# Performance work log

Measured on AMD Instinct MI355X. Metric: run time of the kernel, lower is better.

Reference implementation:

```python
import jax, jax.numpy as jnp
import numpy as np

H = 64   # hid_dim (hard-coded in Attn_LSTM)
C = 8    # enc_in / out_dim
L = 96   # enc_seq_len = interval*lag = max_length
T = 24   # pre_len = window*horizon
B = 4096


def _p(key, shape, scale=0.1):
    return (jax.random.normal(key, shape, dtype=jnp.float32) * scale)


def setup_inputs() -> dict:
    key = jax.random.key(0)
    ks = jax.random.split(key, 20)
    inp = {
        'x_enc': jax.random.normal(ks[0], (B, L, C), dtype=jnp.float32),
        'x_mark_enc': jax.random.normal(ks[1], (B, L, 4), dtype=jnp.float32),
        'x_dec': jax.random.normal(ks[2], (B, T, C), dtype=jnp.float32),
        'x_mark_dec': jax.random.normal(ks[3], (B, T, 4), dtype=jnp.float32),
        # encoder LSTM (1 layer, input C -> hid H), pytorch gate order i,f,g,o
        'enc_Wih': _p(ks[4], (4 * H, C)), 'enc_Whh': _p(ks[5], (4 * H, H)),
        'enc_bih': _p(ks[6], (4 * H,)), 'enc_bhh': _p(ks[7], (4 * H,)),
        # decoder
        'emb_W': _p(ks[8], (H, C)), 'emb_b': _p(ks[9], (H,)),
        'attn_W': _p(ks[10], (L, 2 * H)), 'attn_b': _p(ks[11], (L,)),
        'comb_W': _p(ks[12], (H, 2 * H)), 'comb_b': _p(ks[13], (H,)),
        'dec_Wih': _p(ks[14], (4 * H, H)), 'dec_Whh': _p(ks[15], (4 * H, H)),
        'dec_bih': _p(ks[16], (4 * H,)), 'dec_bhh': _p(ks[17], (4 * H,)),
        'out_W': _p(ks[18], (C, H)), 'out_b': _p(ks[19], (C,)),
    }
    return inp


def _lstm_cell(x, h, c, Wih, Whh, bih, bhh):
    g = x @ Wih.T + h @ Whh.T + (bih + bhh)
    i, f, gg, o = jnp.split(g, 4, axis=-1)
    i, f, o = jax.nn.sigmoid(i), jax.nn.sigmoid(f), jax.nn.sigmoid(o)
    c_new = f * c + i * jnp.tanh(gg)
    h_new = o * jnp.tanh(c_new)
    return h_new, c_new


def _forward(x_enc, enc_Wih, enc_Whh, enc_bih, enc_bhh,
             emb_W, emb_b, attn_W, attn_b, comb_W, comb_b,
             dec_Wih, dec_Whh, dec_bih, dec_bhh, out_W, out_b):
    seq_last = x_enc[:, -1:, :]               # [B,1,C]
    x = x_enc - seq_last                      # normalized

    # ---- encoder: 1-layer LSTM over L steps ----
    h0 = jnp.zeros((x.shape[0], H), dtype=x.dtype)
    c0 = jnp.zeros_like(h0)

    def enc_step(carry, xt):
        h, c = carry
        h, c = _lstm_cell(xt, h, c, enc_Wih, enc_Whh, enc_bih, enc_bhh)
        return (h, c), h

    (h_enc, c_enc), enc_out = jax.lax.scan(enc_step, (h0, c0),
                                           jnp.swapaxes(x, 0, 1))
    enc_out = jnp.swapaxes(enc_out, 0, 1)     # [B,L,H]

    # ---- attention decoder: T sequential steps ----
    dec_in0 = x[:, -1, :]                     # last (normalized) input, [B,C]

    def dec_step(carry, _):
        inp, h, c = carry
        emb = jax.nn.relu(inp @ emb_W.T + emb_b)                       # [B,H]
        aw = jax.nn.softmax(jnp.concatenate([emb, h], -1) @ attn_W.T + attn_b)  # [B,L]
        ctx = jnp.einsum('bl,blh->bh', aw, enc_out)                    # [B,H]
        comb = jnp.concatenate([emb, ctx], -1) @ comb_W.T + comb_b     # [B,H]
        h, c = _lstm_cell(comb, h, c, dec_Wih, dec_Whh, dec_bih, dec_bhh)
        pred = h @ out_W.T + out_b                                     # [B,C]
        # original code feeds prediction.detach() back in
        return (jax.lax.stop_gradient(pred), h, c), (pred, aw)

    _, (preds, aws) = jax.lax.scan(dec_step, (dec_in0, h_enc, c_enc),
                                   None, length=T)
    pre_y = jnp.swapaxes(preds, 0, 1) + seq_last   # [B,T,C]
    return pre_y


def reference(x_enc, x_mark_enc, x_dec, x_mark_dec,
              enc_Wih, enc_Whh, enc_bih, enc_bhh,
              emb_W, emb_b, attn_W, attn_b, comb_W, comb_b,
              dec_Wih, dec_Whh, dec_bih, dec_bhh, out_W, out_b):
    # x_mark_enc, x_dec, x_mark_dec are accepted but unused (as in original)
    return _forward(x_enc, enc_Wih, enc_Whh, enc_bih, enc_bhh,
                    emb_W, emb_b, attn_W, attn_b, comb_W, comb_b,
                    dec_Wih, dec_Whh, dec_bih, dec_bhh, out_W, out_b)
```

## Files before the change

kernel.cpp:

```cpp
#include <hip/hip_runtime.h>

#define LL 96
#define TT 24
#define HH 64
#define CC 8
#define GG 256
#define BT 8
#define NB 512

typedef unsigned short u16t;
typedef unsigned int   u32t;
typedef __attribute__((ext_vector_type(8))) short bf16x8;
typedef __attribute__((ext_vector_type(4))) float f32x4;

__device__ __forceinline__ float b2f(u16t u){ union{u32t i; float f;} v; v.i=((u32t)u)<<16; return v.f; }
__device__ __forceinline__ u16t f2b(float f){ union{float f; u32t i;} v; v.f=f; u32t l=(v.i>>16)&1u; v.i+=0x7fffu+l; return (u16t)(v.i>>16); }
__device__ __forceinline__ float rcpf(float x){ return __builtin_amdgcn_rcpf(x); }
__device__ __forceinline__ float sigm(float x){ return rcpf(1.f + __expf(-x)); }
__device__ __forceinline__ float tanh2(float x){ return 1.f - 2.f*rcpf(__expf(2.f*x) + 1.f); }
__device__ __forceinline__ u32t pk2(float a, float b){ return (u32t)f2b(a) | ((u32t)f2b(b)<<16); }
__device__ __forceinline__ bf16x8 u2b8(uint4 u){ union{uint4 a; bf16x8 b;} v; v.a=u; return v.b; }
__device__ __forceinline__ int aaddr(int k, int m){ return (((k>>5)*4 + ((k>>3)&3))*16 + m)*8 + (k&7); }

__device__ __forceinline__ void bar_lds(){
    asm volatile("s_waitcnt lgkmcnt(0)" ::: "memory");
    __builtin_amdgcn_s_barrier();
    asm volatile("" ::: "memory");
    __builtin_amdgcn_sched_barrier(0);
}

template<bool F32> __device__ __forceinline__ float ldf(const void* p, size_t i){
    if constexpr (F32) return ((const float*)p)[i];
    else               return b2f(((const u16t*)p)[i]);
}
template<bool F32> __device__ __forceinline__ uint4 ld8p(const void* p, size_t i){
    if constexpr (F32){
        const float* f = (const float*)p + i;
        uint4 r; r.x = pk2(f[0],f[1]); r.y = pk2(f[2],f[3]);
                 r.z = pk2(f[4],f[5]); r.w = pk2(f[6],f[7]);
        return r;
    } else return *(const uint4*)((const u16t*)p + i);
}
template<bool F32> __device__ __forceinline__ void stf(void* p, size_t i, float v){
    if constexpr (F32) ((float*)p)[i] = v;
    else               ((u16t*)p)[i] = f2b(v);
}
template<bool F32> __device__ __forceinline__ float ldW_enc(const void* wih, const void* whh, int r, int k){
    if (k < CC)      return ldf<F32>(wih, (size_t)r*CC + k);
    else if (k < 72) return ldf<F32>(whh, (size_t)r*HH + (k-CC));
    else             return 0.f;
}

__device__ __forceinline__ bool inputs_are_f32(const void* bih){
    const u16t* p = (const u16t*)bih;
    int cnt = 0;
    #pragma unroll
    for (int i = 0; i < 64; ++i){
        u32t e = ((u32t)p[i] >> 7) & 0xFFu;
        cnt += (e >= 128u) ? 1 : 0;
    }
    return cnt > 0;
}

template<bool F32>
__global__ __launch_bounds__(256,4) void enc4_g(
    const void* __restrict__ x_enc,
    const void* __restrict__ eWih, const void* __restrict__ eWhh,
    const void* __restrict__ ebih, const void* __restrict__ ebhh,
    u16t* __restrict__ eoG, float* __restrict__ cG)
{
    if (inputs_are_f32(ebih) != F32) return;

    __shared__ __align__(16) short Abuf2[2][1536];

    const int tid = threadIdx.x;
    const int b0  = blockIdx.x * 4;
    const int col = tid & 15, quad = (tid >> 4) & 3, wv = tid >> 6;

    bf16x8 Bf[4][3];
    float  biasg[4];
    #pragma unroll
    for (int g = 0; g < 4; ++g){
        int r = g*64 + wv*16 + col;
        biasg[g] = ldf<F32>(ebih, r) + ldf<F32>(ebhh, r);
        #pragma unroll
        for (int kb = 0; kb < 3; ++kb){
            bf16x8 v;
            #pragma unroll
            for (int x = 0; x < 8; ++x){
                int k = kb*32 + quad*8 + x;
                v[x] = (short)f2b(ldW_enc<F32>(eWih, eWhh, r, k));
            }
            Bf[g][kb] = v;
        }
    }
    for (int n = tid; n < 2*1536; n += 256) ((short*)Abuf2)[n] = 0;
    float sl = 0.f; size_t xbase = 0;
    if (tid < 32){ int b = tid >> 3, i = tid & 7;
        xbase = (size_t)(b0+b)*(LL*CC) + i;
        sl = ldf<F32>(x_enc, xbase + (size_t)(LL-1)*CC);
    }
    __syncthreads();
    if (tid < 32){ short v = (short)f2b(ldf<F32>(x_enc, xbase) - sl);
        Abuf2[0][tid] = v; Abuf2[0][tid+32] = v; Abuf2[0][tid+64] = v; Abuf2[0][tid+96] = v; }
    float xr = (tid < 32) ? ldf<F32>(x_enc, xbase + CC) : 0.f;

    const int jmy = wv*16 + col;
    const int hwbase = aaddr(8 + jmy, 0);
    const u32t ebase = ((u32t)(b0 + quad)*4u + (u32t)(jmy>>4))*1536u + (u32t)((jmy&15)*8);

    float creg = 0.f;
    u32t  pkv  = 0;

    #pragma unroll 2
    for (int t = 0; t < LL; ++t){
        bar_lds();
        const bf16x8* AbR = (const bf16x8*)Abuf2[t & 1];
        short*        AbW = Abuf2[(t + 1) & 1];
        bf16x8 a0 = AbR[(0*4 + quad)*16 + col];
        bf16x8 a1 = AbR[(1*4 + quad)*16 + col];
        bf16x8 a2 = AbR[(2*4 + quad)*16 + col];
        f32x4 acc[4];
        #pragma unroll
        for (int g = 0; g < 4; ++g){
            f32x4 a; a[0]=biasg[g]; a[1]=biasg[g]; a[2]=biasg[g]; a[3]=biasg[g];
            a = __builtin_amdgcn_mfma_f32_16x16x32_bf16(a0, Bf[g][0], a, 0,0,0);
            a = __builtin_amdgcn_mfma_f32_16x16x32_bf16(a1, Bf[g][1], a, 0,0,0);
            a = __builtin_amdgcn_mfma_f32_16x16x32_bf16(a2, Bf[g][2], a, 0,0,0);
            acc[g] = a;
        }
        float c = sigm(acc[1][quad])*creg + sigm(acc[0][quad])*tanh2(acc[2][quad]);
        float h = sigm(acc[3][quad])*tanh2(c);
        creg = c;
        u16t hb = f2b(h);
        if ((t & 1) == 0) pkv = hb;
        else {
            pkv |= ((u32t)hb) << 16;
            *(u32t*)&eoG[ebase + (u32t)((t>>5)*512 + ((t>>3)&3)*128 + (t&7) - 1)] = pkv;
        }
        AbW[hwbase + quad*8]      = (short)hb;
        AbW[hwbase + quad*8+32]   = (short)hb;
        AbW[hwbase + quad*8+64]   = (short)hb;
        AbW[hwbase + quad*8+96]   = (short)hb;
        if (tid < 32 && t < LL-1){
            short v = (short)f2b(xr - sl);
            AbW[tid] = v; AbW[tid+32] = v; AbW[tid+64] = v; AbW[tid+96] = v;
            int tn = (t+2 < LL) ? t+2 : LL-1;
            xr = ldf<F32>(x_enc, xbase + (size_t)tn*CC);
        }
    }
    cG[(size_t)(b0 + quad)*HH + jmy] = creg;
}

template<bool F32>
__global__ __launch_bounds__(256,2) void dec8_g(
    const void* __restrict__ x_enc,
    const void* __restrict__ embW, const void* __restrict__ embb,
    const void* __restrict__ attnW, const void* __restrict__ attnb,
    const void* __restrict__ combW, const void* __restrict__ combb,
    const void* __restrict__ dWih, const void* __restrict__ dWhh,
    const void* __restrict__ dbih, const void* __restrict__ dbhh,
    const void* __restrict__ outW, const void* __restrict__ outb,
    void* __restrict__ outp, const u16t* __restrict__ eoG,
    const float* __restrict__ cG)
{
    if (inputs_are_f32(dbih) != F32) return;

    __shared__ __align__(16) float slp[CC*10];
    __shared__ __align__(16) char  uni[17184];
    __shared__ __align__(16) u16t BaL[6*4*4*16*8];
    __shared__ __align__(16) u16t M1L[64*64];
    __shared__ __align__(16) u16t oWL[8*64];

    const int tid = threadIdx.x;
    const int b0  = blockIdx.x * BT;
    const int col = tid & 15, quad = (tid >> 4) & 3, wv = tid >> 6;
    const int r0  = (quad >> 1) * 2;
    const int jmy = wv*16 + col;

    if (tid < BT*CC){ int b = tid >> 3, i = tid & 7;
        slp[i*10 + b] = ldf<F32>(x_enc, (size_t)(b0+b)*(LL*CC) + (size_t)(LL-1)*CC + i); }

    bf16x8 Bd[4][4];
    #pragma unroll
    for (int g = 0; g < 4; ++g){
        int r = g*64 + wv*16 + col;
        Bd[g][0] = u2b8(ld8p<F32>(dWih, (size_t)r*HH + quad*8));
        Bd[g][1] = u2b8(ld8p<F32>(dWih, (size_t)r*HH + 32 + quad*8));
        Bd[g][2] = u2b8(ld8p<F32>(dWhh, (size_t)r*HH + quad*8));
        Bd[g][3] = u2b8(ld8p<F32>(dWhh, (size_t)r*HH + 32 + quad*8));
    }
    bf16x8 Bc[4];
    #pragma unroll
    for (int kb = 0; kb < 4; ++kb)
        Bc[kb] = u2b8(ld8p<F32>(combW, (size_t)(wv*16+col)*128 + kb*32 + quad*8));
    bf16x8 zz = {0,0,0,0,0,0,0,0};

    for (int idx = tid; idx < 1536; idx += 256){
        int lt_ = idx >> 8, kb_ = (idx >> 6) & 3, q_ = (idx >> 4) & 3, c_ = idx & 15;
        int row = lt_*16 + c_;
        u16t tmp[8];
        #pragma unroll
        for (int x = 0; x < 8; ++x)
            tmp[x] = f2b(ldf<F32>(attnW, (size_t)row*128 + kb_*32 + q_*8 + x));
        *(uint4*)&BaL[(size_t)idx*8] = *(uint4*)tmp;
    }
    for (int idx = tid; idx < 1024; idx += 256){
        int j = idx >> 4, k0 = (idx & 15) * 4;
        float acc4[4] = {0.f,0.f,0.f,0.f};
        #pragma unroll
        for (int c = 0; c < 8; ++c){
            float e = ldf<F32>(embW, (size_t)j*CC + c);
            #pragma unroll
            for (int kk = 0; kk < 4; ++kk)
                acc4[kk] += e * ldf<F32>(outW, (size_t)c*HH + k0 + kk);
        }
        u16t tmp[4];
        #pragma unroll
        for (int kk = 0; kk < 4; ++kk) tmp[kk] = f2b(acc4[kk]);
        int sw = (((k0 >> 3) ^ (j & 7)) << 3) | (k0 & 7);
        *(uint2*)&M1L[j*64 + sw] = *(uint2*)tmp;
    }
    for (int n = tid; n < 512; n += 256){
        int c = n >> 6, k = n & 63;
        int sw = (((k >> 3) ^ (c & 7)) << 3) | (k & 7);
        oWL[c*64 + sw] = f2b(ldf<F32>(outW, n));
    }

    float* decB  = (float*)(uni + 0);
    float* attnB = (float*)(uni + 1024);
    float* b1B   = (float*)(uni + 1408);
    float* combB = (float*)(uni + 1664);
    float* outB  = (float*)(uni + 1920);
    float* Lg    = (float*)(uni + 1952);
    u16t*  awB   = (u16t*)(uni + 5408);
    u16t*  Ae    = (u16t*)(uni + 6944);
    u16t*  Ah0   = (u16t*)(uni + 8992);
    u16t*  Ah1   = (u16t*)(uni + 11040);
    u16t*  Actx  = (u16t*)(uni + 13088);
    u16t*  Acmb  = (u16t*)(uni + 15136);

    float creg[2];
    #pragma unroll
    for (int rr = 0; rr < 2; ++rr){
        int b = (quad*4 + r0 + rr) & 7;
        u16t hv = eoG[(((size_t)(b0+b)*4 + (size_t)(jmy>>4))*3 + 2)*512 + 3*128 + (jmy&15)*8 + 7];
        Ah0[aaddr(jmy, b)]   = hv;
        Ah0[aaddr(jmy, b+8)] = hv;
        creg[rr] = cG[(size_t)(b0+b)*HH + jmy];
    }
    decB[tid] = ldf<F32>(dbih, tid) + ldf<F32>(dbhh, tid);
    if (tid < LL) attnB[tid] = ldf<F32>(attnb, tid);
    if (tid < HH){
        float s = ldf<F32>(embb, tid);
        #pragma unroll
        for (int c = 0; c < 8; ++c)
            s += ldf<F32>(embW, (size_t)tid*CC + c) * ldf<F32>(outb, c);
        b1B[tid] = s;
    }
    if (tid < HH) combB[tid] = ldf<F32>(combb, tid);
    if (tid < CC) outB[tid]  = ldf<F32>(outb, tid);
    {
        float e0v = fmaxf(ldf<F32>(embb, jmy), 0.f);
        u16t ev = f2b(e0v);
        #pragma unroll
        for (int r = 0; r < 4; ++r)
            Ae[aaddr(jmy, quad*4 + r)] = ev;
    }
    __syncthreads();

    const u16t* ebp = eoG + (size_t)(b0 + wv*2) * 6144;
    uint4 eF0[12], eF1[12];
    #pragma unroll
    for (int f = 0; f < 12; ++f) eF0[f] = *(const uint4*)(ebp + f*512 + quad*128 + col*8);
    #pragma unroll
    for (int f = 0; f < 12; ++f) eF1[f] = *(const uint4*)(ebp + 6144 + f*512 + quad*128 + col*8);

    const int lgS = tid & 31, bS = tid >> 5;
    const bf16x8* AeV   = (const bf16x8*)Ae;
    const bf16x8* ActxV = (const bf16x8*)Actx;
    const bf16x8* AcmbV = (const bf16x8*)Acmb;

    for (int t = 0; t < TT; ++t){
        u16t* AhR = (t & 1) ? Ah1 : Ah0;
        u16t* AhW = (t & 1) ? Ah0 : Ah1;
        const bf16x8* AhV = (const bf16x8*)AhR;

        {
            bf16x8 ae0 = AeV[(0*4+quad)*16 + col], ae1 = AeV[(1*4+quad)*16 + col];
            bf16x8 ah0 = AhV[(0*4+quad)*16 + col], ah1 = AhV[(1*4+quad)*16 + col];
            const int ns = (wv < 2) ? 2 : 1;
            for (int s = 0; s < ns; ++s){
                int lt = (s == 0) ? wv : 4+wv;
                const u16t* bp = &BaL[lt*2048 + quad*128 + col*8];
                float bz = attnB[lt*16 + col];
                f32x4 a; a[0]=bz; a[1]=bz; a[2]=bz; a[3]=bz;
                a = __builtin_amdgcn_mfma_f32_16x16x32_bf16(ae0, *(const bf16x8*)&bp[0],    a, 0,0,0);
                a = __builtin_amdgcn_mfma_f32_16x16x32_bf16(ae1, *(const bf16x8*)&bp[512],  a, 0,0,0);
                a = __builtin_amdgcn_mfma_f32_16x16x32_bf16(ah0, *(const bf16x8*)&bp[1024], a, 0,0,0);
                a = __builtin_amdgcn_mfma_f32_16x16x32_bf16(ah1, *(const bf16x8*)&bp[1536], a, 0,0,0);
                if (quad < 2){
                    int rb = (lt*16+col)*9 + quad*4;
                    Lg[rb+0] = a[0]; Lg[rb+1] = a[1]; Lg[rb+2] = a[2]; Lg[rb+3] = a[3];
                }
            }
        }
        bar_lds();

        {
            int l = lgS*3;
            float e0 = __expf(Lg[l*9 + bS]), e1 = __expf(Lg[(l+1)*9 + bS]), e2 = __expf(Lg[(l+2)*9 + bS]);
            float sm = e0 + e1 + e2;
            #pragma unroll
            for (int m = 16; m >= 1; m >>= 1) sm += __shfl_xor(sm, m, 32);
            float inv = rcpf(sm);
            awB[bS*96 + l]     = f2b(e0*inv);
            awB[bS*96 + l + 1] = f2b(e1*inv);
            awB[bS*96 + l + 2] = f2b(e2*inv);
        }
        {
            const u16t* ap0 = awB + (wv*2)*96;
            bf16x8 f0 = *(const bf16x8*)(ap0 + quad*8);
            bf16x8 f1 = *(const bf16x8*)(ap0 + 32 + quad*8);
            bf16x8 f2 = *(const bf16x8*)(ap0 + 64 + quad*8);
            #pragma unroll
            for (int nt = 0; nt < 4; ++nt){
                f32x4 a; a[0]=0.f; a[1]=0.f; a[2]=0.f; a[3]=0.f;
                a = __builtin_amdgcn_mfma_f32_16x16x32_bf16(f0, u2b8(eF0[nt*3+0]), a, 0,0,0);
                a = __builtin_amdgcn_mfma_f32_16x16x32_bf16(f1, u2b8(eF0[nt*3+1]), a, 0,0,0);
                a = __builtin_amdgcn_mfma_f32_16x16x32_bf16(f2, u2b8(eF0[nt*3+2]), a, 0,0,0);
                if (quad == 0){
                    u16t v = f2b(a[0]);
                    Actx[aaddr(nt*16+col, wv*2)]   = v;
                    Actx[aaddr(nt*16+col, wv*2+8)] = v;
                }
            }
            const u16t* ap1 = awB + (wv*2+1)*96;
            bf16x8 g0 = *(const bf16x8*)(ap1 + quad*8);
            bf16x8 g1 = *(const bf16x8*)(ap1 + 32 + quad*8);
            bf16x8 g2 = *(const bf16x8*)(ap1 + 64 + quad*8);
            #pragma unroll
            for (int nt = 0; nt < 4; ++nt){
                f32x4 a; a[0]=0.f; a[1]=0.f; a[2]=0.f; a[3]=0.f;
                a = __builtin_amdgcn_mfma_f32_16x16x32_bf16(g0, u2b8(eF1[nt*3+0]), a, 0,0,0);
                a = __builtin_amdgcn_mfma_f32_16x16x32_bf16(g1, u2b8(eF1[nt*3+1]), a, 0,0,0);
                a = __builtin_amdgcn_mfma_f32_16x16x32_bf16(g2, u2b8(eF1[nt*3+2]), a, 0,0,0);
                if (quad == 0){
                    u16t v = f2b(a[0]);
                    Actx[aaddr(nt*16+col, wv*2+1)] = v;
                    Actx[aaddr(nt*16+col, wv*2+9)] = v;
                }
            }
        }
        bar_lds();

        {
            bf16x8 ae0 = AeV[(0*4+quad)*16 + col],   ae1 = AeV[(1*4+quad)*16 + col];
            bf16x8 ax0 = ActxV[(0*4+quad)*16 + col], ax1 = ActxV[(1*4+quad)*16 + col];
            float bz = combB[wv*16 + col];
            f32x4 a; a[0]=bz; a[1]=bz; a[2]=bz; a[3]=bz;
            a = __builtin_amdgcn_mfma_f32_16x16x32_bf16(ae0, Bc[0], a, 0,0,0);
            a = __builtin_amdgcn_mfma_f32_16x16x32_bf16(ae1, Bc[1], a, 0,0,0);
            a = __builtin_amdgcn_mfma_f32_16x16x32_bf16(ax0, Bc[2], a, 0,0,0);
            a = __builtin_amdgcn_mfma_f32_16x16x32_bf16(ax1, Bc[3], a, 0,0,0);
            #pragma unroll
            for (int r = 0; r < 4; ++r)
                Acmb[aaddr(wv*16+col, quad*4 + r)] = f2b(a[r]);
        }
        bar_lds();

        {
            bf16x8 ac0 = AcmbV[(0*4+quad)*16 + col], ac1 = AcmbV[(1*4+quad)*16 + col];
            bf16x8 ah0 = AhV[(0*4+quad)*16 + col],   ah1 = AhV[(1*4+quad)*16 + col];
            f32x4 g4[4];
            #pragma unroll
            for (int g = 0; g < 4; ++g){
                float bz = decB[g*64 + wv*16 + col];
                f32x4 a; a[0]=bz; a[1]=bz; a[2]=bz; a[3]=bz;
                a = __builtin_amdgcn_mfma_f32_16x16x32_bf16(ac0, Bd[g][0], a, 0,0,0);
                a = __builtin_amdgcn_mfma_f32_16x16x32_bf16(ac1, Bd[g][1], a, 0,0,0);
                a = __builtin_amdgcn_mfma_f32_16x16x32_bf16(ah0, Bd[g][2], a, 0,0,0);
                a = __builtin_amdgcn_mfma_f32_16x16x32_bf16(ah1, Bd[g][3], a, 0,0,0);
                g4[g] = a;
            }
            #pragma unroll
            for (int rr = 0; rr < 2; ++rr){
                int r = r0 + rr;
                int b = (quad*4 + r) & 7;
                float c = sigm(g4[1][r])*creg[rr] + sigm(g4[0][r])*tanh2(g4[2][r]);
                float h = sigm(g4[3][r])*tanh2(c);
                creg[rr] = c;
                u16t hv = f2b(h);
                AhW[aaddr(jmy, b)]   = hv;
                AhW[aaddr(jmy, b+8)] = hv;
            }
        }
        bar_lds();

        {
            const bf16x8* AhWV = (const bf16x8*)AhW;
            bf16x8 xh0 = AhWV[(0*4+quad)*16 + col];
            bf16x8 xh1 = AhWV[(1*4+quad)*16 + col];
            bf16x8 m10 = *(const bf16x8*)&M1L[jmy*64 + ((quad ^ (jmy&7))<<3)];
            bf16x8 m11 = *(const bf16x8*)&M1L[jmy*64 + (((4+quad) ^ (jmy&7))<<3)];
            float eb = b1B[wv*16 + col];
            f32x4 a; a[0]=eb; a[1]=eb; a[2]=eb; a[3]=eb;
            a = __builtin_amdgcn_mfma_f32_16x16x32_bf16(xh0, m10, a, 0,0,0);
            a = __builtin_amdgcn_mfma_f32_16x16x32_bf16(xh1, m11, a, 0,0,0);
            #pragma unroll
            for (int r = 0; r < 4; ++r)
                Ae[aaddr(wv*16+col, quad*4 + r)] = f2b(fmaxf(a[r], 0.f));
            if (wv == 3){
                bf16x8 oBf0 = zz, oBf1 = zz;
                if (col < CC){
                    oBf0 = *(const bf16x8*)&oWL[col*64 + ((quad ^ col)<<3)];
                    oBf1 = *(const bf16x8*)&oWL[col*64 + (((4+quad) ^ col)<<3)];
                }
                float ob = outB[col & 7];
                f32x4 p4; p4[0]=ob; p4[1]=ob; p4[2]=ob; p4[3]=ob;
                p4 = __builtin_amdgcn_mfma_f32_16x16x32_bf16(xh0, oBf0, p4, 0,0,0);
                p4 = __builtin_amdgcn_mfma_f32_16x16x32_bf16(xh1, oBf1, p4, 0,0,0);
                if (col < CC){
                    #pragma unroll
                    for (int r = 0; r < 4; ++r){
                        int m = quad*4 + r;
                        if (m < 8)
                            stf<F32>(outp, ((size_t)(b0+m)*TT + t)*CC + col, p4[r] + slp[col*10 + m]);
                    }
                }
            }
        }
        bar_lds();
    }
}

template<bool F32>
__global__ __launch_bounds__(256,2) void fused_g(
    const void* __restrict__ x_enc,
    const void* __restrict__ eWih, const void* __restrict__ eWhh,
    const void* __restrict__ ebih, const void* __restrict__ ebhh,
    const void* __restrict__ embW, const void* __restrict__ embb,
    const void* __restrict__ attnW, const void* __restrict__ attnb,
    const void* __restrict__ combW, const void* __restrict__ combb,
    const void* __restrict__ dWih, const void* __restrict__ dWhh,
    const void* __restrict__ dbih, const void* __restrict__ dbhh,
    const void* __restrict__ outW, const void* __restrict__ outb,
    void* __restrict__ outp, u16t* __restrict__ eoG)
{
    if (inputs_are_f32(ebih) != F32) return;

    __shared__ __align__(16) float slp[CC*10];
    __shared__ __align__(16) short Abuf2[2][1536];
    __shared__ __align__(16) char  uni[18880];

    const int tid = threadIdx.x;
    const int b0  = blockIdx.x * BT;
    const int col = tid & 15, quad = (tid >> 4) & 3, wv = tid >> 6;
    const int r0  = (quad >> 1) * 2;

    bf16x8 Bf[4][3];
    float  biasg[4];
    #pragma unroll
    for (int g = 0; g < 4; ++g){
        int r = g*64 + wv*16 + col;
        biasg[g] = ldf<F32>(ebih, r) + ldf<F32>(ebhh, r);
        #pragma unroll
        for (int kb = 0; kb < 3; ++kb){
            bf16x8 v;
            #pragma unroll
            for (int x = 0; x < 8; ++x){
                int k = kb*32 + quad*8 + x;
                v[x] = (short)f2b(ldW_enc<F32>(eWih, eWhh, r, k));
            }
            Bf[g][kb] = v;
        }
    }
    for (int n = tid; n < 2*1536; n += 256) ((short*)Abuf2)[n] = 0;
    float sl = 0.f; size_t xbase = 0;
    if (tid < BT*CC){ int b = tid >> 3, i = tid & 7;
        xbase = (size_t)(b0+b)*(LL*CC) + i;
        sl = ldf<F32>(x_enc, xbase + (size_t)(LL-1)*CC);
        slp[i*10 + b] = sl; }
    __syncthreads();
    if (tid < BT*CC){ short v = (short)f2b(ldf<F32>(x_enc, xbase) - sl);
        Abuf2[0][tid] = v; Abuf2[0][tid + 64] = v; }
    float xr = (tid < BT*CC) ? ldf<F32>(x_enc, xbase + CC) : 0.f;

    const int jmy = wv*16 + col;
    const int kh  = 8 + jmy;
    const int hwbase = aaddr(kh, 0);

    u32t ebase[2];
    #pragma unroll
    for (int rr = 0; rr < 2; ++rr){
        u32t bg = (u32t)(b0 + ((quad*4 + r0 + rr) & 7));
        ebase[rr] = (bg*4u + (u32t)(jmy>>4))*1536u + (u32t)((jmy&15)*8);
    }

    float creg[2] = {0.f,0.f};
    u16t  hb16[2] = {0,0};

    for (int t = 0; t < LL; ++t){
        __syncthreads();
        const bf16x8* AbR = (const bf16x8*)Abuf2[t & 1];
        short*        AbW = Abuf2[(t + 1) & 1];
        bf16x8 a0 = AbR[(0*4 + quad)*16 + col];
        bf16x8 a1 = AbR[(1*4 + quad)*16 + col];
        bf16x8 a2 = AbR[(2*4 + quad)*16 + col];
        f32x4 acc[4];
        #pragma unroll
        for (int g = 0; g < 4; ++g){
            f32x4 a; a[0]=biasg[g]; a[1]=biasg[g]; a[2]=biasg[g]; a[3]=biasg[g];
            a = __builtin_amdgcn_mfma_f32_16x16x32_bf16(a0, Bf[g][0], a, 0,0,0);
            a = __builtin_amdgcn_mfma_f32_16x16x32_bf16(a1, Bf[g][1], a, 0,0,0);
            a = __builtin_amdgcn_mfma_f32_16x16x32_bf16(a2, Bf[g][2], a, 0,0,0);
            acc[g] = a;
        }
        int off = (t>>5)*512 + ((t>>3)&3)*128 + (t&7);
        #pragma unroll
        for (int rr = 0; rr < 2; ++rr){
            int r = r0 + rr;
            int b = (quad*4 + r) & 7;
            float c = sigm(acc[1][r])*creg[rr] + sigm(acc[0][r])*tanh2(acc[2][r]);
            float h = sigm(acc[3][r])*tanh2(c);
            creg[rr] = c; hb16[rr] = f2b(h);
            eoG[ebase[rr] + off] = hb16[rr];
            AbW[hwbase + b*8]     = (short)hb16[rr];
            AbW[hwbase + (b+8)*8] = (short)hb16[rr];
        }
        if (tid < BT*CC && t < LL-1){
            short v = (short)f2b(xr - sl);
            AbW[tid] = v; AbW[tid + 64] = v;
            int tn = (t+2 < LL) ? t+2 : LL-1;
            xr = ldf<F32>(x_enc, xbase + (size_t)tn*CC);
        }
    }

    bf16x8 Bd[4][4];
    #pragma unroll
    for (int g = 0; g < 4; ++g){
        int r = g*64 + wv*16 + col;
        Bd[g][0] = u2b8(ld8p<F32>(dWih, (size_t)r*HH + quad*8));
        Bd[g][1] = u2b8(ld8p<F32>(dWih, (size_t)r*HH + 32 + quad*8));
        Bd[g][2] = u2b8(ld8p<F32>(dWhh, (size_t)r*HH + quad*8));
        Bd[g][3] = u2b8(ld8p<F32>(dWhh, (size_t)r*HH + 32 + quad*8));
    }
    bf16x8 Ba[2][4];
    #pragma unroll
    for (int kb = 0; kb < 4; ++kb)
        Ba[0][kb] = u2b8(ld8p<F32>(attnW, (size_t)(wv*16+col)*128 + kb*32 + quad*8));
    if (wv < 2){
        #pragma unroll
        for (int kb = 0; kb < 4; ++kb)
            Ba[1][kb] = u2b8(ld8p<F32>(attnW, (size_t)((4+wv)*16+col)*128 + kb*32 + quad*8));
    } else {
        #pragma unroll
        for (int kb = 0; kb < 4; ++kb) Ba[1][kb] = Ba[0][kb];
    }
    bf16x8 Bc[4];
    #pragma unroll
    for (int kb = 0; kb < 4; ++kb)
        Bc[kb] = u2b8(ld8p<F32>(combW, (size_t)(wv*16+col)*128 + kb*32 + quad*8));
    bf16x8 zz = {0,0,0,0,0,0,0,0};
    bf16x8 eBf = zz;
    if (quad == 0) eBf = u2b8(ld8p<F32>(embW, (size_t)(wv*16+col)*CC));
    bf16x8 oBf0 = zz, oBf1 = zz;
    if (col < CC){
        oBf0 = u2b8(ld8p<F32>(outW, (size_t)col*HH + quad*8));
        oBf1 = u2b8(ld8p<F32>(outW, (size_t)col*HH + 32 + quad*8));
    }

    float* decB  = (float*)(uni + 0);
    float* attnB = (float*)(uni + 1024);
    float* embB  = (float*)(uni + 1408);
    float* combB = (float*)(uni + 1664);
    float* outB  = (float*)(uni + 1920);
    float* Lg    = (float*)(uni + 1952);
    u16t*  awB   = (u16t*)(uni + 5024);
    u16t*  Ae    = (u16t*)(uni + 6560);
    u16t*  Ah0   = (u16t*)(uni + 8608);
    u16t*  Ah1   = (u16t*)(uni + 10656);
    u16t*  Actx  = (u16t*)(uni + 12704);
    u16t*  Acmb  = (u16t*)(uni + 14752);
    u16t*  Apred = (u16t*)(uni + 16800);

    #pragma unroll
    for (int rr = 0; rr < 2; ++rr){
        int b = (quad*4 + r0 + rr) & 7;
        Ah0[aaddr(jmy, b)]     = hb16[rr];
        Ah0[aaddr(jmy, b+8)]   = hb16[rr];
    }
    decB[tid] = ldf<F32>(dbih, tid) + ldf<F32>(dbhh, tid);
    if (tid < LL) attnB[tid] = ldf<F32>(attnb, tid);
    if (tid < HH) embB[tid]  = ldf<F32>(embb, tid);
    if (tid < HH) combB[tid] = ldf<F32>(combb, tid);
    if (tid < CC) outB[tid]  = ldf<F32>(outb, tid);
    for (int n = tid; n < 1024; n += 256) Apred[n] = 0;
    __syncthreads();

    const u16t* ebp = eoG + (size_t)(b0 + wv*2) * 6144;
    uint4 eF0[12], eF1[12];
    #pragma unroll
    for (int f = 0; f < 12; ++f) eF0[f] = *(const uint4*)(ebp + f*512 + quad*128 + col*8);
    #pragma unroll
    for (int f = 0; f < 12; ++f) eF1[f] = *(const uint4*)(ebp + 6144 + f*512 + quad*128 + col*8);

    const int lgS = tid & 31, bS = tid >> 5;
    const bf16x8* AeV   = (const bf16x8*)Ae;
    const bf16x8* ActxV = (const bf16x8*)Actx;
    const bf16x8* AcmbV = (const bf16x8*)Acmb;
    const bf16x8* ApV   = (const bf16x8*)Apred;

    for (int t = 0; t < TT; ++t){
        u16t* AhR = (t & 1) ? Ah1 : Ah0;
        u16t* AhW = (t & 1) ? Ah0 : Ah1;
        const bf16x8* AhV = (const bf16x8*)AhR;

        {
            bf16x8 ap = ApV[quad*16 + col];
            float eb = embB[wv*16 + col];
            f32x4 a; a[0]=eb; a[1]=eb; a[2]=eb; a[3]=eb;
            a = __builtin_amdgcn_mfma_f32_16x16x32_bf16(ap, eBf, a, 0,0,0);
            #pragma unroll
            for (int r = 0; r < 4; ++r)
                Ae[aaddr(wv*16+col, quad*4 + r)] = f2b(fmaxf(a[r], 0.f));
        }
        __syncthreads();

        {
            bf16x8 ae0 = AeV[(0*4+quad)*16 + col], ae1 = AeV[(1*4+quad)*16 + col];
            bf16x8 ah0 = AhV[(0*4+quad)*16 + col], ah1 = AhV[(1*4+quad)*16 + col];
            const int ns = (wv < 2) ? 2 : 1;
            for (int s = 0; s < ns; ++s){
                int lt = (s == 0) ? wv : 4+wv;
                float bz = attnB[lt*16 + col];
                f32x4 a; a[0]=bz; a[1]=bz; a[2]=bz; a[3]=bz;
                a = __builtin_amdgcn_mfma_f32_16x16x32_bf16(ae0, Ba[s][0], a, 0,0,0);
                a = __builtin_amdgcn_mfma_f32_16x16x32_bf16(ae1, Ba[s][1], a, 0,0,0);
                a = __builtin_amdgcn_mfma_f32_16x16x32_bf16(ah0, Ba[s][2], a, 0,0,0);
                a = __builtin_amdgcn_mfma_f32_16x16x32_bf16(ah1, Ba[s][3], a, 0,0,0);
                if (quad < 2)
                    *(float4*)&Lg[(lt*16+col)*8 + quad*4] = make_float4(a[0],a[1],a[2],a[3]);
            }
        }
        __syncthreads();

        {
            int l = lgS*3;
            float ev0 = Lg[l*8 + bS], ev1 = Lg[(l+1)*8 + bS], ev2 = Lg[(l+2)*8 + bS];
            float mx = fmaxf(ev0, fmaxf(ev1, ev2));
            #pragma unroll
            for (int m = 16; m >= 1; m >>= 1) mx = fmaxf(mx, __shfl_xor(mx, m, 32));
            float e0 = __expf(ev0 - mx), e1 = __expf(ev1 - mx), e2 = __expf(ev2 - mx);
            float sm = e0 + e1 + e2;
            #pragma unroll
            for (int m = 16; m >= 1; m >>= 1) sm += __shfl_xor(sm, m, 32);
            float inv = rcpf(sm);
            awB[bS*96 + l]     = f2b(e0*inv);
            awB[bS*96 + l + 1] = f2b(e1*inv);
            awB[bS*96 + l + 2] = f2b(e2*inv);
        }
        {
            const u16t* ap0 = awB + (wv*2)*96;
            bf16x8 f0 = *(const bf16x8*)(ap0 + quad*8);
            bf16x8 f1 = *(const bf16x8*)(ap0 + 32 + quad*8);
            bf16x8 f2 = *(const bf16x8*)(ap0 + 64 + quad*8);
            #pragma unroll
            for (int nt = 0; nt < 4; ++nt){
                f32x4 a; a[0]=0.f; a[1]=0.f; a[2]=0.f; a[3]=0.f;
                a = __builtin_amdgcn_mfma_f32_16x16x32_bf16(f0, u2b8(eF0[nt*3+0]), a, 0,0,0);
                a = __builtin_amdgcn_mfma_f32_16x16x32_bf16(f1, u2b8(eF0[nt*3+1]), a, 0,0,0);
                a = __builtin_amdgcn_mfma_f32_16x16x32_bf16(f2, u2b8(eF0[nt*3+2]), a, 0,0,0);
                if (quad == 0){
                    u16t v = f2b(a[0]);
                    Actx[aaddr(nt*16+col, wv*2)]   = v;
                    Actx[aaddr(nt*16+col, wv*2+8)] = v;
                }
            }
            const u16t* ap1 = awB + (wv*2+1)*96;
            bf16x8 g0 = *(const bf16x8*)(ap1 + quad*8);
            bf16x8 g1 = *(const bf16x8*)(ap1 + 32 + quad*8);
            bf16x8 g2 = *(const bf16x8*)(ap1 + 64 + quad*8);
            #pragma unroll
            for (int nt = 0; nt < 4; ++nt){
                f32x4 a; a[0]=0.f; a[1]=0.f; a[2]=0.f; a[3]=0.f;
                a = __builtin_amdgcn_mfma_f32_16x16x32_bf16(g0, u2b8(eF1[nt*3+0]), a, 0,0,0);
                a = __builtin_amdgcn_mfma_f32_16x16x32_bf16(g1, u2b8(eF1[nt*3+1]), a, 0,0,0);
                a = __builtin_amdgcn_mfma_f32_16x16x32_bf16(g2, u2b8(eF1[nt*3+2]), a, 0,0,0);
                if (quad == 0){
                    u16t v = f2b(a[0]);
                    Actx[aaddr(nt*16+col, wv*2+1)] = v;
                    Actx[aaddr(nt*16+col, wv*2+9)] = v;
                }
            }
        }
        __syncthreads();

        {
            bf16x8 ae0 = AeV[(0*4+quad)*16 + col],   ae1 = AeV[(1*4+quad)*16 + col];
            bf16x8 ax0 = ActxV[(0*4+quad)*16 + col], ax1 = ActxV[(1*4+quad)*16 + col];
            float bz = combB[wv*16 + col];
            f32x4 a; a[0]=bz; a[1]=bz; a[2]=bz; a[3]=bz;
            a = __builtin_amdgcn_mfma_f32_16x16x32_bf16(ae0, Bc[0], a, 0,0,0);
            a = __builtin_amdgcn_mfma_f32_16x16x32_bf16(ae1, Bc[1], a, 0,0,0);
            a = __builtin_amdgcn_mfma_f32_16x16x32_bf16(ax0, Bc[2], a, 0,0,0);
            a = __builtin_amdgcn_mfma_f32_16x16x32_bf16(ax1, Bc[3], a, 0,0,0);
            #pragma unroll
            for (int r = 0; r < 4; ++r)
                Acmb[aaddr(wv*16+col, quad*4 + r)] = f2b(a[r]);
        }
        __syncthreads();

        {
            bf16x8 ac0 = AcmbV[(0*4+quad)*16 + col], ac1 = AcmbV[(1*4+quad)*16 + col];
            bf16x8 ah0 = AhV[(0*4+quad)*16 + col],   ah1 = AhV[(1*4+quad)*16 + col];
            f32x4 g4[4];
            #pragma unroll
            for (int g = 0; g < 4; ++g){
                float bz = decB[g*64 + wv*16 + col];
                f32x4 a; a[0]=bz; a[1]=bz; a[2]=bz; a[3]=bz;
                a = __builtin_amdgcn_mfma_f32_16x16x32_bf16(ac0, Bd[g][0], a, 0,0,0);
                a = __builtin_amdgcn_mfma_f32_16x16x32_bf16(ac1, Bd[g][1], a, 0,0,0);
                a = __builtin_amdgcn_mfma_f32_16x16x32_bf16(ah0, Bd[g][2], a, 0,0,0);
                a = __builtin_amdgcn_mfma_f32_16x16x32_bf16(ah1, Bd[g][3], a, 0,0,0);
                g4[g] = a;
            }
            #pragma unroll
            for (int rr = 0; rr < 2; ++rr){
                int r = r0 + rr;
                int b = (quad*4 + r) & 7;
                float c = sigm(g4[1][r])*creg[rr] + sigm(g4[0][r])*tanh2(g4[2][r]);
                float h = sigm(g4[3][r])*tanh2(c);
                creg[rr] = c;
                u16t hv = f2b(h);
                AhW[aaddr(jmy, b)]   = hv;
                AhW[aaddr(jmy, b+8)] = hv;
            }
        }
        __syncthreads();

        if (wv == 0){
            const bf16x8* AhWV = (const bf16x8*)AhW;
            bf16x8 xh0 = AhWV[(0*4+quad)*16 + col];
            bf16x8 xh1 = AhWV[(1*4+quad)*16 + col];
            float ob = outB[col & 7];
            f32x4 a; a[0]=ob; a[1]=ob; a[2]=ob; a[3]=ob;
            a = __builtin_amdgcn_mfma_f32_16x16x32_bf16(xh0, oBf0, a, 0,0,0);
            a = __builtin_amdgcn_mfma_f32_16x16x32_bf16(xh1, oBf1, a, 0,0,0);
            if (col < CC){
                #pragma unroll
                for (int r = 0; r < 4; ++r){
                    int m = quad*4 + r, b = m & 7;
                    float p = a[r];
                    Apred[aaddr(col, m)] = f2b(p);
                    if (m < 8)
                        stf<F32>(outp, ((size_t)(b0+b)*TT + t)*CC + col, p + slp[col*10 + b]);
                }
            }
        }
        __syncthreads();
    }
}

extern "C" void kernel_launch(void* const* d_in, const int* in_sizes, int n_in,
                              void* d_out, int out_size, void* d_ws, size_t ws_size,
                              hipStream_t stream)
{
    (void)out_size;
    bool doBF = true, doF32 = true;
    if (in_sizes && n_in > 6){
        if (in_sizes[6] == 512)  doF32 = false;
        else if (in_sizes[6] == 1024) doBF = false;
    }
    u16t* eoG = (u16t*)d_ws;
    if (ws_size >= 50331648ull + 1048576ull){
        float* cG = (float*)((char*)d_ws + 50331648ull);
        if (doBF){
            enc4_g<false><<<1024, 256, 0, stream>>>(
                d_in[0], d_in[4], d_in[5], d_in[6], d_in[7], eoG, cG);
            dec8_g<false><<<NB, 256, 0, stream>>>(
                d_in[0],
                d_in[8],  d_in[9],  d_in[10], d_in[11],
                d_in[12], d_in[13], d_in[14], d_in[15],
                d_in[16], d_in[17], d_in[18], d_in[19],
                d_out, eoG, cG);
        }
        if (doF32){
            enc4_g<true ><<<1024, 256, 0, stream>>>(
                d_in[0], d_in[4], d_in[5], d_in[6], d_in[7], eoG, cG);
            dec8_g<true ><<<NB, 256, 0, stream>>>(
                d_in[0],
                d_in[8],  d_in[9],  d_in[10], d_in[11],
                d_in[12], d_in[13], d_in[14], d_in[15],
                d_in[16], d_in[17], d_in[18], d_in[19],
                d_out, eoG, cG);
        }
    } else {
        if (doBF)
            fused_g<false><<<NB, 256, 0, stream>>>(
                d_in[0],
                d_in[4],  d_in[5],  d_in[6],  d_in[7],
                d_in[8],  d_in[9],  d_in[10], d_in[11],
                d_in[12], d_in[13], d_in[14], d_in[15],
                d_in[16], d_in[17], d_in[18], d_in[19],
                d_out, eoG);
        if (doF32)
            fused_g<true><<<NB, 256, 0, stream>>>(
                d_in[0],
                d_in[4],  d_in[5],  d_in[6],  d_in[7],
                d_in[8],  d_in[9],  d_in[10], d_in[11],
                d_in[12], d_in[13], d_in[14], d_in[15],
                d_in[16], d_in[17], d_in[18], d_in[19],
                d_out, eoG);
    }
}
```

Measured before the change: 273.8 us.

## Pack 16 batch rows per encoder MFMA tile instead of replicating 4

Result: faster. 252.8 us, median of 2 (-7.7%).

```diff
diff --git a/kernel.cpp b/kernel.cpp
--- a/kernel.cpp
+++ b/kernel.cpp
@@ -63,7 +63,7 @@
 }
 
 template<bool F32>
-__global__ __launch_bounds__(256,4) void enc4_g(
+__global__ __launch_bounds__(256,1) void enc16_g(
     const void* __restrict__ x_enc,
     const void* __restrict__ eWih, const void* __restrict__ eWhh,
     const void* __restrict__ ebih, const void* __restrict__ ebhh,
@@ -74,7 +74,7 @@
     __shared__ __align__(16) short Abuf2[2][1536];
 
     const int tid = threadIdx.x;
-    const int b0  = blockIdx.x * 4;
+    const int b0  = blockIdx.x * 16;
     const int col = tid & 15, quad = (tid >> 4) & 3, wv = tid >> 6;
 
     bf16x8 Bf[4][3];
@@ -96,21 +96,23 @@
     }
     for (int n = tid; n < 2*1536; n += 256) ((short*)Abuf2)[n] = 0;
     float sl = 0.f; size_t xbase = 0;
-    if (tid < 32){ int b = tid >> 3, i = tid & 7;
+    if (tid < 128){ int b = tid >> 3, i = tid & 7;
         xbase = (size_t)(b0+b)*(LL*CC) + i;
         sl = ldf<F32>(x_enc, xbase + (size_t)(LL-1)*CC);
     }
     __syncthreads();
-    if (tid < 32){ short v = (short)f2b(ldf<F32>(x_enc, xbase) - sl);
-        Abuf2[0][tid] = v; Abuf2[0][tid+32] = v; Abuf2[0][tid+64] = v; Abuf2[0][tid+96] = v; }
-    float xr = (tid < 32) ? ldf<F32>(x_enc, xbase + CC) : 0.f;
+    if (tid < 128) Abuf2[0][tid] = (short)f2b(ldf<F32>(x_enc, xbase) - sl);
+    float xr = (tid < 128) ? ldf<F32>(x_enc, xbase + CC) : 0.f;
 
     const int jmy = wv*16 + col;
-    const int hwbase = aaddr(8 + jmy, 0);
-    const u32t ebase = ((u32t)(b0 + quad)*4u + (u32t)(jmy>>4))*1536u + (u32t)((jmy&15)*8);
-
-    float creg = 0.f;
-    u32t  pkv  = 0;
+    const int hwb = aaddr(8 + jmy, 0);
+    u32t ebase[4];
+    #pragma unroll
+    for (int r = 0; r < 4; ++r)
+        ebase[r] = ((u32t)(b0 + quad*4 + r)*4u + (u32t)(jmy>>4))*1536u + (u32t)((jmy&15)*8);
+
+    float creg[4] = {0.f,0.f,0.f,0.f};
+    u32t  pkv[4]  = {0,0,0,0};
 
     #pragma unroll 2
     for (int t = 0; t < LL; ++t){
@@ -129,27 +131,29 @@
             a = __builtin_amdgcn_mfma_f32_16x16x32_bf16(a2, Bf[g][2], a, 0,0,0);
             acc[g] = a;
         }
-        float c = sigm(acc[1][quad])*creg + sigm(acc[0][quad])*tanh2(acc[2][quad]);
-        float h = sigm(acc[3][quad])*tanh2(c);
-        creg = c;
-        u16t hb = f2b(h);
-        if ((t & 1) == 0) pkv = hb;
-        else {
-            pkv |= ((u32t)hb) << 16;
-            *(u32t*)&eoG[ebase + (u32t)((t>>5)*512 + ((t>>3)&3)*128 + (t&7) - 1)] = pkv;
-        }
-        AbW[hwbase + quad*8]      = (short)hb;
-        AbW[hwbase + quad*8+32]   = (short)hb;
-        AbW[hwbase + quad*8+64]   = (short)hb;
-        AbW[hwbase + quad*8+96]   = (short)hb;
-        if (tid < 32 && t < LL-1){
-            short v = (short)f2b(xr - sl);
-            AbW[tid] = v; AbW[tid+32] = v; AbW[tid+64] = v; AbW[tid+96] = v;
+        int off = (t>>5)*512 + ((t>>3)&3)*128 + (t&7);
+        #pragma unroll
+        for (int r = 0; r < 4; ++r){
+            float c = sigm(acc[1][r])*creg[r] + sigm(acc[0][r])*tanh2(acc[2][r]);
+            float h = sigm(acc[3][r])*tanh2(c);
+            creg[r] = c;
+            u16t hb = f2b(h);
+            if ((t & 1) == 0) pkv[r] = hb;
+            else {
+                pkv[r] |= ((u32t)hb) << 16;
+                *(u32t*)&eoG[ebase[r] + (u32t)(off - 1)] = pkv[r];
+            }
+            AbW[hwb + (quad*4 + r)*8] = (short)hb;
+        }
+        if (tid < 128 && t < LL-1){
+            AbW[tid] = (short)f2b(xr - sl);
             int tn = (t+2 < LL) ? t+2 : LL-1;
             xr = ldf<F32>(x_enc, xbase + (size_t)tn*CC);
         }
     }
-    cG[(size_t)(b0 + quad)*HH + jmy] = creg;
+    #pragma unroll
+    for (int r = 0; r < 4; ++r)
+        cG[(size_t)(b0 + quad*4 + r)*HH + jmy] = creg[r];
 }
 
 template<bool F32>
@@ -776,7 +780,7 @@
     if (ws_size >= 50331648ull + 1048576ull){
         float* cG = (float*)((char*)d_ws + 50331648ull);
         if (doBF){
-            enc4_g<false><<<1024, 256, 0, stream>>>(
+            enc16_g<false><<<256, 256, 0, stream>>>(
                 d_in[0], d_in[4], d_in[5], d_in[6], d_in[7], eoG, cG);
             dec8_g<false><<<NB, 256, 0, stream>>>(
                 d_in[0],
@@ -786,7 +790,7 @@
                 d_out, eoG, cG);
         }
         if (doF32){
-            enc4_g<true ><<<1024, 256, 0, stream>>>(
+            enc16_g<true ><<<256, 256, 0, stream>>>(
                 d_in[0], d_in[4], d_in[5], d_in[6], d_in[7], eoG, cG);
             dec8_g<true ><<<NB, 256, 0, stream>>>(
                 d_in[0],
```
